# Performance work log

Measured on AMD Instinct MI355X. Metric: run time of the kernel, lower is better.

Reference implementation:

```python
import jax, jax.numpy as jnp
import numpy as np

B, LIN, LOUT = 16, 100, 100
V, D, AD, H, HID = 32000, 512, 64, 8, 2048
RECYCLE, PAD = 1, 0
SCALE = float(np.sqrt(AD))

def _pe(L, dim):
    # positional(pos, i) = pos / 10000 ** ((i//2)/dim); sin on even i, cos on odd i
    pos = jnp.arange(L, dtype=jnp.float32)[:, None]
    i = jnp.arange(dim)
    ang = pos / jnp.power(jnp.float32(10000.0), (i // 2).astype(jnp.float32) / dim)
    return jnp.where(i % 2 == 0, jnp.sin(ang), jnp.cos(ang))  # (L, dim)

def _ln(x, g, b):
    m = x.mean(-1, keepdims=True)
    v = ((x - m) ** 2).mean(-1, keepdims=True)
    return (x - m) / jnp.sqrt(v + 1e-5) * g + b

def _mha(q, k, v, mask, p):
    wq, bq, wk, bk, wv, bv, wo, bo, g, b = p
    m, lq, _ = q.shape
    lk = k.shape[1]
    Q = (q @ wq + bq).reshape(m, lq, H, AD).transpose(0, 2, 1, 3)
    K = (k @ wk + bk).reshape(m, lk, H, AD).transpose(0, 2, 1, 3)
    Vh = (v @ wv + bv).reshape(m, lk, H, AD).transpose(0, 2, 1, 3)
    attn = jnp.einsum('mnld,mnkd->mnlk', Q / SCALE, K)
    attn = jnp.where(mask[:, None, :, :], attn, jnp.float32(-1e9))
    attn = jax.nn.softmax(attn, axis=-1)
    o = jnp.einsum('mnlk,mnkd->mnld', attn, Vh)
    # original uses rearrange 'm n l d -> m l (d n)': d is the OUTER factor
    o = o.transpose(0, 2, 3, 1).reshape(m, lq, AD * H)
    o = o @ wo + bo + q  # dropout is identity in eval
    return _ln(o, g, b)

def _ff(x, w1, b1, w2, b2, g, b):
    return _ln(jax.nn.relu(x @ w1 + b1) @ w2 + b2 + x, g, b)

def _forward(floats, inputs, outputs):
    (sw, fcb,
     ewq, ebq, ewk, ebk, ewv, ebv, ewo, ebo, eg1, eb1, ef1w, ef1b, ef2w, ef2b, eg2, eb2,
     dwq, dbq, dwk, dbk, dwv, dbv, dwo, dbo, dg1, db1, df1w, df1b, df2w, df2b, dg2, db2) = floats
    enc_p = (ewq, ebq, ewk, ebk, ewv, ebv, ewo, ebo, eg1, eb1)
    dec_p = (dwq, dbq, dwk, dbk, dwv, dbv, dwo, dbo, dg1, db1)
    in_mask = (inputs != PAD)[:, None, :]                    # (B,1,LIN) -> bcast (B,1,1,LIN)
    tril = jnp.tril(jnp.ones((LOUT, LOUT), dtype=bool))
    out_mask = (outputs != PAD)[:, None, :] & tril[None]     # (B,LOUT,LOUT)
    enc = sw[inputs] + _pe(LIN, D)[None]
    for _ in range(RECYCLE + 1):  # shared weights reused each iteration
        enc = _mha(enc, enc, enc, in_mask, enc_p)
        enc = _ff(enc, ef1w, ef1b, ef2w, ef2b, eg2, eb2)
    dec = sw[outputs] + _pe(LOUT, D)[None]
    for _ in range(RECYCLE + 1):  # same MHA module for self- and cross-attention
        dec = _mha(dec, dec, dec, out_mask, dec_p)
        dec = _mha(dec, enc, enc, in_mask, dec_p)
        dec = _ff(dec, df1w, df1b, df2w, df2b, dg2, db2)
    dec = dec * jnp.float32(D ** -0.5)
    logits = dec @ sw.T + fcb  # fc.weight tied to share_weight
    return jax.nn.softmax(logits, axis=-1)

def setup_inputs():
    key = jax.random.key(0)
    ks = iter(jax.random.split(key, 64))
    rn = lambda shape: jax.random.normal(next(ks), shape, dtype=jnp.float32) * 0.02
    z = lambda shape: jnp.zeros(shape, jnp.float32)
    o = lambda shape: jnp.ones(shape, jnp.float32)
    d = {'inputs': jax.random.randint(next(ks), (B, LIN), 0, V),
         'outputs': jax.random.randint(next(ks), (B, LOUT), 0, V),
         'share_weight': rn((V, D)), 'fc_b': z((V,))}
    for p in ('enc', 'dec'):
        d[f'{p}_wq'] = rn((D, H * AD)); d[f'{p}_bq'] = z((H * AD,))
        d[f'{p}_wk'] = rn((D, H * AD)); d[f'{p}_bk'] = z((H * AD,))
        d[f'{p}_wv'] = rn((D, H * AD)); d[f'{p}_bv'] = z((H * AD,))
        d[f'{p}_wo'] = rn((H * AD, D)); d[f'{p}_bo'] = z((D,))
        d[f'{p}_g1'] = o((D,)); d[f'{p}_b1'] = z((D,))
        d[f'{p}_f1w'] = rn((D, HID)); d[f'{p}_f1b'] = z((HID,))
        d[f'{p}_f2w'] = rn((HID, D)); d[f'{p}_f2b'] = z((D,))
        d[f'{p}_g2'] = o((D,)); d[f'{p}_b2'] = z((D,))
    return d

def reference(inputs, outputs, share_weight, fc_b, enc_wq, enc_bq, enc_wk, enc_bk, enc_wv, enc_bv, enc_wo, enc_bo, enc_g1, enc_b1, enc_f1w, enc_f1b, enc_f2w, enc_f2b, enc_g2, enc_b2, dec_wq, dec_bq, dec_wk, dec_bk, dec_wv, dec_bv, dec_wo, dec_bo, dec_g1, dec_b1, dec_f1w, dec_f1b, dec_f2w, dec_f2b, dec_g2, dec_b2):
    floats = (share_weight, fc_b, enc_wq, enc_bq, enc_wk, enc_bk, enc_wv, enc_bv, enc_wo, enc_bo, enc_g1, enc_b1, enc_f1w, enc_f1b, enc_f2w, enc_f2b, enc_g2, enc_b2, dec_wq, dec_bq, dec_wk, dec_bk, dec_wv, dec_bv, dec_wo, dec_bo, dec_g1, dec_b1, dec_f1w, dec_f1b, dec_f2w, dec_f2b, dec_g2, dec_b2)
    return _forward(floats, inputs, outputs)
```

## Files before the change

kernel.cpp:

```cpp
#include <hip/hip_runtime.h>

#define TQ     1600
#define MP     1664
#define DM     512
#define NHD    8
#define HD     64
#define VOCAB  32000
#define HID    2048
#define LSEQ   100
#define NSTRIPE 500
#define SCALEV 0.044194173824159216f

typedef unsigned short u16;
typedef unsigned int u32;
typedef __attribute__((ext_vector_type(8))) short bf16x8;
typedef __attribute__((ext_vector_type(4))) float f32x4;

__device__ __forceinline__ u16 f2b(float x) {
  union { float f; unsigned u; } c; c.f = x;
  unsigned r = (c.u + 0x7FFFu + ((c.u >> 16) & 1u)) >> 16;
  return (u16)r;
}
__device__ __forceinline__ float b2f(u16 b) {
  union { unsigned u; float f; } c; c.u = ((unsigned)b) << 16; return c.f;
}
__device__ __forceinline__ unsigned pk2(float lo, float hi) {
  return (unsigned)f2b(lo) | ((unsigned)f2b(hi) << 16);
}
__device__ __forceinline__ float wredsum(float v) {
#pragma unroll
  for (int o = 32; o > 0; o >>= 1) v += __shfl_xor(v, o, 64);
  return v;
}

struct PrepArgs {
  const float* wsrc[12];
  u16* wdst[12];
  int K[12], N[12], toff[12];
  int ntile;
  const float* bsrc[6];
  float* qbE; float* qbD;
};

__global__ __launch_bounds__(256) void prep_kernel(PrepArgs a) {
  __shared__ float t[64][65];
  int bid = blockIdx.x, tid = threadIdx.x;
  if (bid < a.ntile) {
    int wi = 0;
#pragma unroll
    for (int i = 1; i < 12; ++i) if (bid >= a.toff[i]) wi = i;
    int tile = bid - a.toff[wi];
    int K = a.K[wi], N = a.N[wi];
    int ktiles = K >> 6;
    int k0 = (tile % ktiles) << 6, n0 = (tile / ktiles) << 6;
    const float* src = a.wsrc[wi];
    u16* dst = a.wdst[wi];
    int r = tid >> 4, c = (tid & 15) * 4;
#pragma unroll
    for (int i = 0; i < 4; ++i) {
      float4 v = *(const float4*)(src + (size_t)(k0 + r + i * 16) * N + n0 + c);
      t[r + i * 16][c + 0] = v.x; t[r + i * 16][c + 1] = v.y;
      t[r + i * 16][c + 2] = v.z; t[r + i * 16][c + 3] = v.w;
    }
    __syncthreads();
#pragma unroll
    for (int i = 0; i < 4; ++i) {
      int n = r + i * 16;
      ushort4 o;
      o.x = f2b(t[c + 0][n]); o.y = f2b(t[c + 1][n]);
      o.z = f2b(t[c + 2][n]); o.w = f2b(t[c + 3][n]);
      *(ushort4*)(dst + (size_t)(n0 + n) * K + k0 + c) = o;
    }
  } else {
    int j = (bid - a.ntile) * 256 + tid;
    if (j < 3072) {
      int which = j >> 9, o = j & 511;
      float v = a.bsrc[which][o];
      if (which < 3) a.qbE[which * 512 + o] = v;
      else           a.qbD[(which - 3) * 512 + o] = v;
    }
  }
}

__global__ __launch_bounds__(256) void embed_kernel(const int* __restrict__ tokA,
                                                    const int* __restrict__ tokB,
                                                    const float* __restrict__ sw,
                                                    u16* __restrict__ bufA,
                                                    u16* __restrict__ bufB) {
  const int half = MP * DM / 256;
  int bid = blockIdx.x;
  const int* tok = (bid < half) ? tokA : tokB;
  u16* out = (bid < half) ? bufA : bufB;
  int idx = (bid < half ? bid : bid - half) * 256 + threadIdx.x;
  int row = idx >> 9, d = idx & 511;
  float v = 0.f;
  if (row < TQ) {
    int l = row % LSEQ;
    int t = tok[row];
    float freq = expf(-(float)(d >> 1) * (9.210340371976184f / 512.0f));
    float ang = (float)l * freq;
    float pe = (d & 1) ? cosf(ang) : sinf(ang);
    v = sw[(size_t)t * DM + d] + pe;
  }
  out[idx] = f2b(v);
}

template<bool RELU, bool RES>
__global__ __launch_bounds__(256) void bgemm_kernel(
    const u16* __restrict__ A, const u16* __restrict__ BT,
    const float* __restrict__ bias, const u16* __restrict__ res,
    u16* __restrict__ C, int K, int ldc)
{
  __shared__ u16 As[64 * 64];
  __shared__ u16 Bs[64 * 64];
  const int tid = threadIdx.x;
  const int m0 = blockIdx.y << 6, n0 = blockIdx.x << 6;
  const int w = tid >> 6, lane = tid & 63;
  const int c = lane & 15, q = lane >> 4;
  const int srow = tid >> 2, sc = tid & 3;
  const int xr = (srow & 7) << 4;
  const u16* ag = A + (size_t)(m0 + srow) * K + sc * 16;
  const u16* bg = BT + (size_t)(n0 + srow) * K + sc * 16;
  const int arow = w * 16 + c;
  const int axr = (arow & 7) << 4;
  f32x4 acc[4];
#pragma unroll
  for (int t = 0; t < 4; ++t) acc[t] = (f32x4){0.f, 0.f, 0.f, 0.f};

  for (int k0 = 0; k0 < K; k0 += 64) {
    __syncthreads();
    uint4 a0 = *(const uint4*)(ag + k0);
    uint4 a1 = *(const uint4*)(ag + k0 + 8);
    uint4 b0 = *(const uint4*)(bg + k0);
    uint4 b1 = *(const uint4*)(bg + k0 + 8);
    *(uint4*)((char*)As + srow * 128 + ((sc * 32) ^ xr)) = a0;
    *(uint4*)((char*)As + srow * 128 + ((sc * 32 + 16) ^ xr)) = a1;
    *(uint4*)((char*)Bs + srow * 128 + ((sc * 32) ^ xr)) = b0;
    *(uint4*)((char*)Bs + srow * 128 + ((sc * 32 + 16) ^ xr)) = b1;
    __syncthreads();
#pragma unroll
    for (int ks = 0; ks < 2; ++ks) {
      bf16x8 af = *(bf16x8*)((char*)As + arow * 128 + ((ks * 64 + q * 16) ^ axr));
#pragma unroll
      for (int t = 0; t < 4; ++t) {
        int brow = t * 16 + c;
        bf16x8 bf = *(bf16x8*)((char*)Bs + brow * 128 + ((ks * 64 + q * 16) ^ ((brow & 7) << 4)));
        acc[t] = __builtin_amdgcn_mfma_f32_16x16x32_bf16(af, bf, acc[t], 0, 0, 0);
      }
    }
  }
  const int r0 = q * 4;
#pragma unroll
  for (int t = 0; t < 4; ++t) {
    int col = n0 + t * 16 + c;
    float bsv = bias[col];
#pragma unroll
    for (int r = 0; r < 4; ++r) {
      int row = m0 + w * 16 + r0 + r;
      float v = acc[t][r] + bsv;
      if (RES) v += b2f(res[(size_t)row * ldc + col]);
      if (RELU) v = fmaxf(v, 0.f);
      C[(size_t)row * ldc + col] = f2b(v);
    }
  }
}

__global__ __launch_bounds__(256) void ln_kernel(u16* __restrict__ X,
                                                 const float* __restrict__ g,
                                                 const float* __restrict__ b) {
  int row = blockIdx.x * 4 + (threadIdx.x >> 6);
  int lane = threadIdx.x & 63;
  u16* p = X + (size_t)row * DM + lane * 8;
  uint4 u = *(uint4*)p;
  unsigned uu[4] = {u.x, u.y, u.z, u.w};
  float x[8];
#pragma unroll
  for (int e = 0; e < 4; ++e) {
    x[e * 2]     = b2f((u16)(uu[e] & 0xffff));
    x[e * 2 + 1] = b2f((u16)(uu[e] >> 16));
  }
  float s = 0.f;
#pragma unroll
  for (int j = 0; j < 8; ++j) s += x[j];
  s = wredsum(s);
  float mean = s * (1.0f / 512.0f);
  float d2 = 0.f;
#pragma unroll
  for (int j = 0; j < 8; ++j) { float d = x[j] - mean; d2 += d * d; }
  d2 = wredsum(d2);
  float r = rsqrtf(d2 * (1.0f / 512.0f) + 1e-5f);
  const float* gg = g + lane * 8;
  const float* bb = b + lane * 8;
  float y[8];
#pragma unroll
  for (int j = 0; j < 8; ++j) y[j] = (x[j] - mean) * r * gg[j] + bb[j];
  uint4 o;
  o.x = pk2(y[0], y[1]); o.y = pk2(y[2], y[3]);
  o.z = pk2(y[4], y[5]); o.w = pk2(y[6], y[7]);
  *(uint4*)p = o;
}

__global__ __launch_bounds__(256) void attn_kernel(
    const u16* __restrict__ QKV, const int* __restrict__ tok,
    u16* __restrict__ O, int causal)
{
  __shared__ u16 Qs[112 * 64];
  __shared__ u16 Ks[112 * 64];
  __shared__ u16 Vt[64 * 128];
  __shared__ u16 Ps[112 * 128];
  __shared__ int tokv[112];
  int b = blockIdx.x >> 3, h = blockIdx.x & 7;
  int tid = threadIdx.x;

  for (int i = tid; i < 4096; i += 256) ((u32*)Vt)[i] = 0;
  for (int i = tid; i < 7168; i += 256) ((u32*)Ps)[i] = 0;
  if (tid < 112) tokv[tid] = (tid < 100) ? (tok[b * LSEQ + tid] != 0) : 0;
  __syncthreads();

  const size_t rowbase = (size_t)(b * LSEQ) * 1536 + h * 64;
  for (int i = tid; i < 896; i += 256) {
    int r = i >> 3, c8 = i & 7;
    size_t g = rowbase + (size_t)r * 1536 + c8 * 8;
    uint4 q4 = *(const uint4*)(QKV + g);
    uint4 k4 = *(const uint4*)(QKV + g + 512);
    int off = (c8 * 16) ^ ((r & 7) << 4);
    *(uint4*)((char*)Qs + r * 128 + off) = q4;
    *(uint4*)((char*)Ks + r * 128 + off) = k4;
    if (r < LSEQ) {
      union { uint4 u; u16 s[8]; } cv;
      cv.u = *(const uint4*)(QKV + g + 1024);
#pragma unroll
      for (int j = 0; j < 8; ++j) {
        int d = c8 * 8 + j;
        *(u16*)((char*)Vt + d * 256 + ((2 * r) ^ ((d & 7) << 4))) = cv.s[j];
      }
    }
  }
  __syncthreads();

  const int lane = tid & 63, w = tid >> 6;
  const int c = lane & 15, q = lane >> 4;

#pragma unroll
  for (int half = 0; half < 2; ++half) {
    int mt = w + half * 4;
    if (mt > 6) continue;
    f32x4 s[7];
#pragma unroll
    for (int nt = 0; nt < 7; ++nt) s[nt] = (f32x4){0.f, 0.f, 0.f, 0.f};
    int arow = mt * 16 + c;
    int axr = (arow & 7) << 4;
    bf16x8 a0 = *(bf16x8*)((char*)Qs + arow * 128 + ((q * 16) ^ axr));
    bf16x8 a1 = *(bf16x8*)((char*)Qs + arow * 128 + ((64 + q * 16) ^ axr));
#pragma unroll
    for (int nt = 0; nt < 7; ++nt) {
      int brow = nt * 16 + c;
      int bxr = (brow & 7) << 4;
      bf16x8 b0 = *(bf16x8*)((char*)Ks + brow * 128 + ((q * 16) ^ bxr));
      bf16x8 b1 = *(bf16x8*)((char*)Ks + brow * 128 + ((64 + q * 16) ^ bxr));
      s[nt] = __builtin_amdgcn_mfma_f32_16x16x32_bf16(a0, b0, s[nt], 0, 0, 0);
      s[nt] = __builtin_amdgcn_mfma_f32_16x16x32_bf16(a1, b1, s[nt], 0, 0, 0);
    }
#pragma unroll
    for (int r = 0; r < 4; ++r) {
      int mrow = mt * 16 + q * 4 + r;
      float sv[7];
      float mx = -3.0e38f;
#pragma unroll
      for (int nt = 0; nt < 7; ++nt) {
        int kcol = nt * 16 + c;
        float x = s[nt][r];
        bool real = kcol < LSEQ;
        bool ok = real && tokv[kcol] && (!causal || kcol <= mrow);
        x = ok ? x * 0.125f : (real ? -1e9f : -3.0e38f);
        sv[nt] = x;
        mx = fmaxf(mx, x);
      }
#pragma unroll
      for (int o = 1; o < 16; o <<= 1) mx = fmaxf(mx, __shfl_xor(mx, o, 64));
      float sum = 0.f;
#pragma unroll
      for (int nt = 0; nt < 7; ++nt) { sv[nt] = __expf(sv[nt] - mx); sum += sv[nt]; }
#pragma unroll
      for (int o = 1; o < 16; o <<= 1) sum += __shfl_xor(sum, o, 64);
      float inv = 1.0f / sum;
      int pxr = (mrow & 7) << 4;
#pragma unroll
      for (int nt = 0; nt < 7; ++nt) {
        int kcol = nt * 16 + c;
        *(u16*)((char*)Ps + mrow * 256 + ((2 * kcol) ^ pxr)) = f2b(sv[nt] * inv);
      }
    }
    asm volatile("s_waitcnt lgkmcnt(0)" ::: "memory");
    __builtin_amdgcn_sched_barrier(0);
    int prow = mt * 16 + c;
    int pxr2 = (prow & 7) << 4;
    bf16x8 pa[4];
#pragma unroll
    for (int ks = 0; ks < 4; ++ks)
      pa[ks] = *(bf16x8*)((char*)Ps + prow * 256 + ((ks * 64 + q * 16) ^ pxr2));
#pragma unroll
    for (int dt = 0; dt < 4; ++dt) {
      f32x4 o = (f32x4){0.f, 0.f, 0.f, 0.f};
      int vrow = dt * 16 + c;
      int vxr = (vrow & 7) << 4;
#pragma unroll
      for (int ks = 0; ks < 4; ++ks) {
        bf16x8 vb = *(bf16x8*)((char*)Vt + vrow * 256 + ((ks * 64 + q * 16) ^ vxr));
        o = __builtin_amdgcn_mfma_f32_16x16x32_bf16(pa[ks], vb, o, 0, 0, 0);
      }
#pragma unroll
      for (int r = 0; r < 4; ++r) {
        int mrow = mt * 16 + q * 4 + r;
        if (mrow < LSEQ) {
          int d = dt * 16 + c;
          O[(size_t)(b * LSEQ + mrow) * DM + d * 8 + h] = f2b(o[r]);
        }
      }
    }
  }
}

template<bool PART>
__global__ __launch_bounds__(256) void vgemm_kernel(
    const u16* __restrict__ A, const float* __restrict__ sw,
    const float* __restrict__ fcb, float* __restrict__ out,
    float2* __restrict__ pbuf)
{
  __shared__ u16 Bs[64 * 512];
  const int tid = threadIdx.x;
  const int n0 = blockIdx.x << 6;
  for (int i = tid; i < 4096; i += 256) {
    int row = i >> 6, c8 = i & 63;
    const float* s = sw + (size_t)(n0 + row) * DM + c8 * 8;
    float4 f0 = *(const float4*)s;
    float4 f1 = *(const float4*)(s + 4);
    uint4 o;
    o.x = pk2(f0.x, f0.y); o.y = pk2(f0.z, f0.w);
    o.z = pk2(f1.x, f1.y); o.w = pk2(f1.z, f1.w);
    *(uint4*)((char*)Bs + row * 1024 + ((c8 * 16) ^ ((row & 7) << 4))) = o;
  }
  __syncthreads();
  const int w = tid >> 6, lane = tid & 63;
  const int c = lane & 15, q = lane >> 4;
  const u16* pA = A + (size_t)(w * 16 + c) * DM + q * 8;
  float fb[4];
#pragma unroll
  for (int t = 0; t < 4; ++t) fb[t] = fcb[n0 + t * 16 + c];
  for (int mt = 0; mt < 25; ++mt) {
    f32x4 acc[4];
#pragma unroll
    for (int t = 0; t < 4; ++t) acc[t] = (f32x4){0.f, 0.f, 0.f, 0.f};
    size_t moff = (size_t)mt * 64 * DM;
#pragma unroll 4
    for (int ks = 0; ks < 16; ++ks) {
      union { uint4 u; bf16x8 b; } ca;
      ca.u = *(const uint4*)(pA + moff + ks * 32);
#pragma unroll
      for (int t = 0; t < 4; ++t) {
        int brow = t * 16 + c;
        bf16x8 bf = *(bf16x8*)((char*)Bs + brow * 1024 + ((ks * 64 + q * 16) ^ ((brow & 7) << 4)));
        acc[t] = __builtin_amdgcn_mfma_f32_16x16x32_bf16(ca.b, bf, acc[t], 0, 0, 0);
      }
    }
    float lv[4][4];
#pragma unroll
    for (int t = 0; t < 4; ++t)
#pragma unroll
      for (int r = 0; r < 4; ++r) lv[t][r] = acc[t][r] * SCALEV + fb[t];
#pragma unroll
    for (int t = 0; t < 4; ++t) {
      int col = n0 + t * 16 + c;
#pragma unroll
      for (int r = 0; r < 4; ++r) {
        int row = mt * 64 + w * 16 + q * 4 + r;
        out[(size_t)row * VOCAB + col] = lv[t][r];
      }
    }
    if (PART) {
      float pm[4], ps[4];
#pragma unroll
      for (int r = 0; r < 4; ++r) {
        float mx = fmaxf(fmaxf(lv[0][r], lv[1][r]), fmaxf(lv[2][r], lv[3][r]));
#pragma unroll
        for (int o = 1; o < 16; o <<= 1) mx = fmaxf(mx, __shfl_xor(mx, o, 64));
        float ss = 0.f;
#pragma unroll
        for (int t = 0; t < 4; ++t) ss += __expf(lv[t][r] - mx);
#pragma unroll
        for (int o = 1; o < 16; o <<= 1) ss += __shfl_xor(ss, o, 64);
        pm[r] = mx; ps[r] = ss;
      }
      if (c < 4) {
        int row = mt * 64 + w * 16 + q * 4 + c;
        pbuf[(size_t)row * NSTRIPE + blockIdx.x] = make_float2(pm[c], ps[c]);
      }
    }
  }
}

__global__ __launch_bounds__(256) void reduce_partials(const float2* __restrict__ pbuf,
                                                       float2* __restrict__ MS) {
  int row = blockIdx.x * 4 + (threadIdx.x >> 6);
  int lane = threadIdx.x & 63;
  float m = -3.0e38f, s = 0.f;
  for (int i = lane; i < NSTRIPE; i += 64) {
    float2 p = pbuf[(size_t)row * NSTRIPE + i];
    float mn = fmaxf(m, p.x);
    s = s * __expf(m - mn) + p.y * __expf(p.x - mn);
    m = mn;
  }
#pragma unroll
  for (int o = 1; o < 64; o <<= 1) {
    float m2 = __shfl_xor(m, o, 64);
    float s2 = __shfl_xor(s, o, 64);
    float mn = fmaxf(m, m2);
    s = s * __expf(m - mn) + s2 * __expf(m2 - mn);
    m = mn;
  }
  if (lane == 0) MS[row] = make_float2(m, 1.0f / s);
}

__global__ __launch_bounds__(256) void rowstat_kernel(const float* __restrict__ L,
                                                      float2* __restrict__ MS) {
  __shared__ float am[4], as_[4];
  int row = blockIdx.x, tid = threadIdx.x;
  const float* p = L + (size_t)row * VOCAB;
  float m = -3.0e38f, s = 0.f;
  for (int i = tid; i < VOCAB; i += 256) {
    float x = p[i];
    if (x > m) { s *= __expf(m - x); m = x; }
    s += __expf(x - m);
  }
#pragma unroll
  for (int o = 1; o < 64; o <<= 1) {
    float m2 = __shfl_xor(m, o, 64);
    float s2 = __shfl_xor(s, o, 64);
    float mn = fmaxf(m, m2);
    s = s * __expf(m - mn) + s2 * __expf(m2 - mn);
    m = mn;
  }
  if ((tid & 63) == 0) { am[tid >> 6] = m; as_[tid >> 6] = s; }
  __syncthreads();
  if (tid == 0) {
    float M = am[0], S = as_[0];
#pragma unroll
    for (int k = 1; k < 4; ++k) {
      float mn = fmaxf(M, am[k]);
      S = S * __expf(M - mn) + as_[k] * __expf(am[k] - mn);
      M = mn;
    }
    MS[row] = make_float2(M, 1.0f / S);
  }
}

__global__ __launch_bounds__(256) void vfinal_kernel(float* __restrict__ P,
                                                     const float2* __restrict__ MS) {
  int row = blockIdx.y;
  int col = blockIdx.x * 1024 + threadIdx.x * 4;
  if (col >= VOCAB) return;
  float2 ms = MS[row];
  float* p = P + (size_t)row * VOCAB + col;
  float4 x = *(float4*)p;
  x.x = __expf(x.x - ms.x) * ms.y;
  x.y = __expf(x.y - ms.x) * ms.y;
  x.z = __expf(x.z - ms.x) * ms.y;
  x.w = __expf(x.w - ms.x) * ms.y;
  *(float4*)p = x;
}

extern "C" void kernel_launch(void* const* d_in, const int* in_sizes, int n_in,
                              void* d_out, int out_size, void* d_ws, size_t ws_size,
                              hipStream_t stream) {
  (void)in_sizes; (void)n_in; (void)out_size;
  const int* inputs  = (const int*)d_in[0];
  const int* outputs = (const int*)d_in[1];
  const float* sw  = (const float*)d_in[2];
  const float* fcb = (const float*)d_in[3];
  const float* E[16];
  const float* Dd[16];
  for (int i = 0; i < 16; ++i) E[i]  = (const float*)d_in[4 + i];
  for (int i = 0; i < 16; ++i) Dd[i] = (const float*)d_in[20 + i];

  u16* bufE = (u16*)d_ws;
  u16* bufD = bufE + (size_t)MP * DM;
  size_t offMS = (size_t)2 * MP * DM * 2;
  size_t offPB = offMS + (size_t)TQ * 8;
  size_t need  = offPB + (size_t)TQ * NSTRIPE * 8;
  float2* MS   = (float2*)((char*)d_ws + offMS);
  float2* pbuf = (float2*)((char*)d_ws + offPB);
  bool part = ws_size >= need;

  char* base = (char*)d_out;
  size_t off = 0;
  auto carve = [&](size_t bytes) { void* p = base + off; off += (bytes + 255) & ~(size_t)255; return p; };
  u16* bqkvE = (u16*)carve((size_t)MP * 1536 * 2);
  u16* bqkvD = (u16*)carve((size_t)MP * 1536 * 2);
  u16* ba    = (u16*)carve((size_t)MP * DM * 2);
  u16* bh    = (u16*)carve((size_t)MP * HID * 2);
  u16* wqkvE = (u16*)carve((size_t)1536 * 512 * 2);
  u16* woE   = (u16*)carve((size_t)512 * 512 * 2);
  u16* f1E   = (u16*)carve((size_t)2048 * 512 * 2);
  u16* f2E   = (u16*)carve((size_t)512 * 2048 * 2);
  u16* wqkvD = (u16*)carve((size_t)1536 * 512 * 2);
  u16* woD   = (u16*)carve((size_t)512 * 512 * 2);
  u16* f1D   = (u16*)carve((size_t)2048 * 512 * 2);
  u16* f2D   = (u16*)carve((size_t)512 * 2048 * 2);
  float* qbE = (float*)carve(1536 * 4);
  float* qbD = (float*)carve(1536 * 4);
  float* out = (float*)d_out;

  PrepArgs pa;
  const float* ws_[12] = {E[0], E[2], E[4], E[6], E[10], E[12],
                          Dd[0], Dd[2], Dd[4], Dd[6], Dd[10], Dd[12]};
  u16* wd_[12] = {wqkvE, wqkvE + 512 * 512, wqkvE + 1024 * 512, woE, f1E, f2E,
                  wqkvD, wqkvD + 512 * 512, wqkvD + 1024 * 512, woD, f1D, f2D};
  int K_[12] = {512, 512, 512, 512, 512, 2048, 512, 512, 512, 512, 512, 2048};
  int N_[12] = {512, 512, 512, 512, 2048, 512, 512, 512, 512, 512, 2048, 512};
  int tiles = 0;
  for (int i = 0; i < 12; ++i) {
    pa.wsrc[i] = ws_[i]; pa.wdst[i] = wd_[i]; pa.K[i] = K_[i]; pa.N[i] = N_[i];
    pa.toff[i] = tiles;
    tiles += (K_[i] >> 6) * (N_[i] >> 6);
  }
  pa.ntile = tiles;
  const float* bs_[6] = {E[1], E[3], E[5], Dd[1], Dd[3], Dd[5]};
  for (int i = 0; i < 6; ++i) pa.bsrc[i] = bs_[i];
  pa.qbE = qbE; pa.qbD = qbD;
  prep_kernel<<<tiles + 12, 256, 0, stream>>>(pa);

  embed_kernel<<<2 * MP * DM / 256, 256, 0, stream>>>(inputs, outputs, sw, bufE, bufD);

  const dim3 Gqkv(24, 26), G512(8, 26), Gkv(16, 26), Ghid(32, 26);

  for (int it = 0; it < 2; ++it) {
    bgemm_kernel<false,false><<<Gqkv,256,0,stream>>>(bufE, wqkvE, qbE, nullptr, bqkvE, 512, 1536);
    attn_kernel<<<128,256,0,stream>>>(bqkvE, inputs, ba, 0);
    bgemm_kernel<false,true><<<G512,256,0,stream>>>(ba, woE, E[7], bufE, bufE, 512, 512);
    ln_kernel<<<TQ/4,256,0,stream>>>(bufE, E[8], E[9]);
    bgemm_kernel<true,false><<<Ghid,256,0,stream>>>(bufE, f1E, E[11], nullptr, bh, 512, 2048);
    bgemm_kernel<false,true><<<G512,256,0,stream>>>(bh, f2E, E[13], bufE, bufE, 2048, 512);
    ln_kernel<<<TQ/4,256,0,stream>>>(bufE, E[14], E[15]);
  }
  for (int it = 0; it < 2; ++it) {
    bgemm_kernel<false,false><<<Gqkv,256,0,stream>>>(bufD, wqkvD, qbD, nullptr, bqkvD, 512, 1536);
    attn_kernel<<<128,256,0,stream>>>(bqkvD, outputs, ba, 1);
    bgemm_kernel<false,true><<<G512,256,0,stream>>>(ba, woD, Dd[7], bufD, bufD, 512, 512);
    ln_kernel<<<TQ/4,256,0,stream>>>(bufD, Dd[8], Dd[9]);
    bgemm_kernel<false,false><<<G512,256,0,stream>>>(bufD, wqkvD, qbD, nullptr, bqkvD, 512, 1536);
    bgemm_kernel<false,false><<<Gkv,256,0,stream>>>(bufE, wqkvD + 512 * 512, qbD + 512, nullptr, bqkvD + 512, 512, 1536);
    attn_kernel<<<128,256,0,stream>>>(bqkvD, inputs, ba, 0);
    bgemm_kernel<false,true><<<G512,256,0,stream>>>(ba, woD, Dd[7], bufD, bufD, 512, 512);
    ln_kernel<<<TQ/4,256,0,stream>>>(bufD, Dd[8], Dd[9]);
    bgemm_kernel<true,false><<<Ghid,256,0,stream>>>(bufD, f1D, Dd[11], nullptr, bh, 512, 2048);
    bgemm_kernel<false,true><<<G512,256,0,stream>>>(bh, f2D, Dd[13], bufD, bufD, 2048, 512);
    ln_kernel<<<TQ/4,256,0,stream>>>(bufD, Dd[14], Dd[15]);
  }

  if (part) {
    vgemm_kernel<true><<<NSTRIPE, 256, 0, stream>>>(bufD, sw, fcb, out, pbuf);
    reduce_partials<<<TQ / 4, 256, 0, stream>>>(pbuf, MS);
  } else {
    vgemm_kernel<false><<<NSTRIPE, 256, 0, stream>>>(bufD, sw, fcb, out, nullptr);
    rowstat_kernel<<<TQ, 256, 0, stream>>>(out, MS);
  }
  vfinal_kernel<<<dim3(32, TQ), 256, 0, stream>>>(out, MS);
}
```

Baseline: 587.8 us.

## Retile GEMMs, split attention by query half, and recompute vocab logits for softmax

Several changes at once. Large GEMMs get a 128-row tile template. Attention launches twice as many blocks, each handling half the queries. The decoder cross-attention K/V projection of the encoder output is hoisted out of the decoder loop, and the positional table is precomputed in the prep kernel. The vocab projection now processes five row tiles per pass, and in partial mode it recomputes the logits in a second pass that writes the softmax directly, replacing the fp32 logits write plus the separate normalize kernel. The recompute doubles the vocab GEMM's arithmetic in exchange for dropping a full read-modify-write of the large output.

```diff
diff --git a/kernel.cpp b/kernel.cpp
--- a/kernel.cpp
+++ b/kernel.cpp
@@ -39,7 +39,7 @@
   int K[12], N[12], toff[12];
   int ntile;
   const float* bsrc[6];
-  float* qbE; float* qbD;
+  float* qbE; float* qbD; float* peT;
 };
 
 __global__ __launch_bounds__(256) void prep_kernel(PrepArgs a) {
@@ -71,7 +71,7 @@
       o.z = f2b(t[c + 2][n]); o.w = f2b(t[c + 3][n]);
       *(ushort4*)(dst + (size_t)(n0 + n) * K + k0 + c) = o;
     }
-  } else {
+  } else if (bid < a.ntile + 12) {
     int j = (bid - a.ntile) * 256 + tid;
     if (j < 3072) {
       int which = j >> 9, o = j & 511;
@@ -79,12 +79,21 @@
       if (which < 3) a.qbE[which * 512 + o] = v;
       else           a.qbD[(which - 3) * 512 + o] = v;
     }
+  } else {
+    int idx = (bid - a.ntile - 12) * 256 + tid;
+    if (idx < LSEQ * 512) {
+      int l = idx >> 9, d = idx & 511;
+      float freq = expf(-(float)(d >> 1) * (9.210340371976184f / 512.0f));
+      float ang = (float)l * freq;
+      a.peT[idx] = (d & 1) ? cosf(ang) : sinf(ang);
+    }
   }
 }
 
 __global__ __launch_bounds__(256) void embed_kernel(const int* __restrict__ tokA,
                                                     const int* __restrict__ tokB,
                                                     const float* __restrict__ sw,
+                                                    const float* __restrict__ peT,
                                                     u16* __restrict__ bufA,
                                                     u16* __restrict__ bufB) {
   const int half = MP * DM / 256;
@@ -97,67 +106,74 @@
   if (row < TQ) {
     int l = row % LSEQ;
     int t = tok[row];
-    float freq = expf(-(float)(d >> 1) * (9.210340371976184f / 512.0f));
-    float ang = (float)l * freq;
-    float pe = (d & 1) ? cosf(ang) : sinf(ang);
-    v = sw[(size_t)t * DM + d] + pe;
+    v = sw[(size_t)t * DM + d] + peT[l * 512 + d];
   }
   out[idx] = f2b(v);
 }
 
-template<bool RELU, bool RES>
+template<int MT, bool RELU, bool RES>
 __global__ __launch_bounds__(256) void bgemm_kernel(
     const u16* __restrict__ A, const u16* __restrict__ BT,
     const float* __restrict__ bias, const u16* __restrict__ res,
     u16* __restrict__ C, int K, int ldc)
 {
-  __shared__ u16 As[64 * 64];
+  __shared__ u16 As[64 * MT * 64];
   __shared__ u16 Bs[64 * 64];
   const int tid = threadIdx.x;
-  const int m0 = blockIdx.y << 6, n0 = blockIdx.x << 6;
+  const int m0 = blockIdx.y * (64 * MT), n0 = blockIdx.x << 6;
   const int w = tid >> 6, lane = tid & 63;
   const int c = lane & 15, q = lane >> 4;
-  const int srow = tid >> 2, sc = tid & 3;
-  const int xr = (srow & 7) << 4;
-  const u16* ag = A + (size_t)(m0 + srow) * K + sc * 16;
-  const u16* bg = BT + (size_t)(n0 + srow) * K + sc * 16;
-  const int arow = w * 16 + c;
-  const int axr = (arow & 7) << 4;
-  f32x4 acc[4];
-#pragma unroll
-  for (int t = 0; t < 4; ++t) acc[t] = (f32x4){0.f, 0.f, 0.f, 0.f};
+  const int tr = tid >> 3, tc = tid & 7;
+  const int sbase = tr * 128 + ((tc * 16) ^ ((tr & 7) << 4));
+  const u16* agp = A + (size_t)(m0 + tr) * K + tc * 8;
+  const u16* bgp = BT + (size_t)(n0 + tr) * K + tc * 8;
+  f32x4 acc[MT][4];
+#pragma unroll
+  for (int i = 0; i < MT; ++i)
+#pragma unroll
+    for (int t = 0; t < 4; ++t) acc[i][t] = (f32x4){0.f, 0.f, 0.f, 0.f};
 
   for (int k0 = 0; k0 < K; k0 += 64) {
     __syncthreads();
-    uint4 a0 = *(const uint4*)(ag + k0);
-    uint4 a1 = *(const uint4*)(ag + k0 + 8);
-    uint4 b0 = *(const uint4*)(bg + k0);
-    uint4 b1 = *(const uint4*)(bg + k0 + 8);
-    *(uint4*)((char*)As + srow * 128 + ((sc * 32) ^ xr)) = a0;
-    *(uint4*)((char*)As + srow * 128 + ((sc * 32 + 16) ^ xr)) = a1;
-    *(uint4*)((char*)Bs + srow * 128 + ((sc * 32) ^ xr)) = b0;
-    *(uint4*)((char*)Bs + srow * 128 + ((sc * 32 + 16) ^ xr)) = b1;
+#pragma unroll
+    for (int rep = 0; rep < 2 * MT; ++rep) {
+      uint4 v = *(const uint4*)(agp + k0 + (size_t)rep * 32 * K);
+      *(uint4*)((char*)As + sbase + rep * 4096) = v;
+    }
+#pragma unroll
+    for (int rep = 0; rep < 2; ++rep) {
+      uint4 v = *(const uint4*)(bgp + k0 + (size_t)rep * 32 * K);
+      *(uint4*)((char*)Bs + sbase + rep * 4096) = v;
+    }
     __syncthreads();
 #pragma unroll
     for (int ks = 0; ks < 2; ++ks) {
-      bf16x8 af = *(bf16x8*)((char*)As + arow * 128 + ((ks * 64 + q * 16) ^ axr));
+      bf16x8 af[MT];
+#pragma unroll
+      for (int i = 0; i < MT; ++i) {
+        int arow = w * 16 * MT + i * 16 + c;
+        af[i] = *(bf16x8*)((char*)As + arow * 128 + ((ks * 64 + q * 16) ^ ((arow & 7) << 4)));
+      }
 #pragma unroll
       for (int t = 0; t < 4; ++t) {
         int brow = t * 16 + c;
         bf16x8 bf = *(bf16x8*)((char*)Bs + brow * 128 + ((ks * 64 + q * 16) ^ ((brow & 7) << 4)));
-        acc[t] = __builtin_amdgcn_mfma_f32_16x16x32_bf16(af, bf, acc[t], 0, 0, 0);
-      }
-    }
-  }
-  const int r0 = q * 4;
+#pragma unroll
+        for (int i = 0; i < MT; ++i)
+          acc[i][t] = __builtin_amdgcn_mfma_f32_16x16x32_bf16(af[i], bf, acc[i][t], 0, 0, 0);
+      }
+    }
+  }
+#pragma unroll
+  for (int i = 0; i < MT; ++i)
 #pragma unroll
   for (int t = 0; t < 4; ++t) {
     int col = n0 + t * 16 + c;
     float bsv = bias[col];
 #pragma unroll
     for (int r = 0; r < 4; ++r) {
-      int row = m0 + w * 16 + r0 + r;
-      float v = acc[t][r] + bsv;
+      int row = m0 + w * 16 * MT + i * 16 + q * 4 + r;
+      float v = acc[i][t][r] + bsv;
       if (RES) v += b2f(res[(size_t)row * ldc + col]);
       if (RELU) v = fmaxf(v, 0.f);
       C[(size_t)row * ldc + col] = f2b(v);
@@ -204,16 +220,17 @@
     const u16* __restrict__ QKV, const int* __restrict__ tok,
     u16* __restrict__ O, int causal)
 {
-  __shared__ u16 Qs[112 * 64];
+  __shared__ u16 Qs[64 * 64];
   __shared__ u16 Ks[112 * 64];
   __shared__ u16 Vt[64 * 128];
-  __shared__ u16 Ps[112 * 128];
+  __shared__ u16 Ps[64 * 128];
   __shared__ int tokv[112];
-  int b = blockIdx.x >> 3, h = blockIdx.x & 7;
+  int bid = blockIdx.x;
+  int b = bid >> 4, h = (bid >> 1) & 7, half = bid & 1;
   int tid = threadIdx.x;
 
   for (int i = tid; i < 4096; i += 256) ((u32*)Vt)[i] = 0;
-  for (int i = tid; i < 7168; i += 256) ((u32*)Ps)[i] = 0;
+  for (int i = tid; i < 4096; i += 256) ((u32*)Ps)[i] = 0;
   if (tid < 112) tokv[tid] = (tid < 100) ? (tok[b * LSEQ + tid] != 0) : 0;
   __syncthreads();
 
@@ -221,11 +238,13 @@
   for (int i = tid; i < 896; i += 256) {
     int r = i >> 3, c8 = i & 7;
     size_t g = rowbase + (size_t)r * 1536 + c8 * 8;
-    uint4 q4 = *(const uint4*)(QKV + g);
+    int off = (c8 * 16) ^ ((r & 7) << 4);
     uint4 k4 = *(const uint4*)(QKV + g + 512);
-    int off = (c8 * 16) ^ ((r & 7) << 4);
-    *(uint4*)((char*)Qs + r * 128 + off) = q4;
     *(uint4*)((char*)Ks + r * 128 + off) = k4;
+    if (r < 64) {
+      uint4 q4 = *(const uint4*)(QKV + g + (size_t)(half * 64) * 1536);
+      *(uint4*)((char*)Qs + r * 128 + off) = q4;
+    }
     if (r < LSEQ) {
       union { uint4 u; u16 s[8]; } cv;
       cv.u = *(const uint4*)(QKV + g + 1024);
@@ -240,11 +259,9 @@
 
   const int lane = tid & 63, w = tid >> 6;
   const int c = lane & 15, q = lane >> 4;
-
-#pragma unroll
-  for (int half = 0; half < 2; ++half) {
-    int mt = w + half * 4;
-    if (mt > 6) continue;
+  const int mt = w;
+  const int mbase = half * 64 + mt * 16;
+  if (mbase < 112) {
     f32x4 s[7];
 #pragma unroll
     for (int nt = 0; nt < 7; ++nt) s[nt] = (f32x4){0.f, 0.f, 0.f, 0.f};
@@ -263,7 +280,8 @@
     }
 #pragma unroll
     for (int r = 0; r < 4; ++r) {
-      int mrow = mt * 16 + q * 4 + r;
+      int mrow = mbase + q * 4 + r;
+      int ml = mt * 16 + q * 4 + r;
       float sv[7];
       float mx = -3.0e38f;
 #pragma unroll
@@ -284,11 +302,11 @@
 #pragma unroll
       for (int o = 1; o < 16; o <<= 1) sum += __shfl_xor(sum, o, 64);
       float inv = 1.0f / sum;
-      int pxr = (mrow & 7) << 4;
+      int pxr = (ml & 7) << 4;
 #pragma unroll
       for (int nt = 0; nt < 7; ++nt) {
         int kcol = nt * 16 + c;
-        *(u16*)((char*)Ps + mrow * 256 + ((2 * kcol) ^ pxr)) = f2b(sv[nt] * inv);
+        *(u16*)((char*)Ps + ml * 256 + ((2 * kcol) ^ pxr)) = f2b(sv[nt] * inv);
       }
     }
     asm volatile("s_waitcnt lgkmcnt(0)" ::: "memory");
@@ -311,7 +329,7 @@
       }
 #pragma unroll
       for (int r = 0; r < 4; ++r) {
-        int mrow = mt * 16 + q * 4 + r;
+        int mrow = mbase + q * 4 + r;
         if (mrow < LSEQ) {
           int d = dt * 16 + c;
           O[(size_t)(b * LSEQ + mrow) * DM + d * 8 + h] = f2b(o[r]);
@@ -321,11 +339,11 @@
   }
 }
 
-template<bool PART>
+template<int MODE>
 __global__ __launch_bounds__(256) void vgemm_kernel(
     const u16* __restrict__ A, const float* __restrict__ sw,
     const float* __restrict__ fcb, float* __restrict__ out,
-    float2* __restrict__ pbuf)
+    float2* __restrict__ pbuf, const float2* __restrict__ MS)
 {
   __shared__ u16 Bs[64 * 512];
   const int tid = threadIdx.x;
@@ -343,57 +361,75 @@
   __syncthreads();
   const int w = tid >> 6, lane = tid & 63;
   const int c = lane & 15, q = lane >> 4;
-  const u16* pA = A + (size_t)(w * 16 + c) * DM + q * 8;
   float fb[4];
 #pragma unroll
   for (int t = 0; t < 4; ++t) fb[t] = fcb[n0 + t * 16 + c];
-  for (int mt = 0; mt < 25; ++mt) {
-    f32x4 acc[4];
-#pragma unroll
-    for (int t = 0; t < 4; ++t) acc[t] = (f32x4){0.f, 0.f, 0.f, 0.f};
-    size_t moff = (size_t)mt * 64 * DM;
+
+  for (int g = 0; g < 5; ++g) {
+    f32x4 acc[5][4];
+#pragma unroll
+    for (int j = 0; j < 5; ++j)
+#pragma unroll
+      for (int t = 0; t < 4; ++t) acc[j][t] = (f32x4){0.f, 0.f, 0.f, 0.f};
+    const u16* pA = A + (size_t)(g * 320 + w * 16 + c) * DM + q * 8;
 #pragma unroll 4
     for (int ks = 0; ks < 16; ++ks) {
-      union { uint4 u; bf16x8 b; } ca;
-      ca.u = *(const uint4*)(pA + moff + ks * 32);
+      union { uint4 u; bf16x8 b; } ca[5];
+#pragma unroll
+      for (int j = 0; j < 5; ++j)
+        ca[j].u = *(const uint4*)(pA + (size_t)j * 64 * DM + ks * 32);
 #pragma unroll
       for (int t = 0; t < 4; ++t) {
         int brow = t * 16 + c;
         bf16x8 bf = *(bf16x8*)((char*)Bs + brow * 1024 + ((ks * 64 + q * 16) ^ ((brow & 7) << 4)));
-        acc[t] = __builtin_amdgcn_mfma_f32_16x16x32_bf16(ca.b, bf, acc[t], 0, 0, 0);
-      }
-    }
-    float lv[4][4];
-#pragma unroll
-    for (int t = 0; t < 4; ++t)
-#pragma unroll
-      for (int r = 0; r < 4; ++r) lv[t][r] = acc[t][r] * SCALEV + fb[t];
-#pragma unroll
-    for (int t = 0; t < 4; ++t) {
-      int col = n0 + t * 16 + c;
-#pragma unroll
-      for (int r = 0; r < 4; ++r) {
-        int row = mt * 64 + w * 16 + q * 4 + r;
-        out[(size_t)row * VOCAB + col] = lv[t][r];
-      }
-    }
-    if (PART) {
-      float pm[4], ps[4];
-#pragma unroll
-      for (int r = 0; r < 4; ++r) {
-        float mx = fmaxf(fmaxf(lv[0][r], lv[1][r]), fmaxf(lv[2][r], lv[3][r]));
-#pragma unroll
-        for (int o = 1; o < 16; o <<= 1) mx = fmaxf(mx, __shfl_xor(mx, o, 64));
-        float ss = 0.f;
-#pragma unroll
-        for (int t = 0; t < 4; ++t) ss += __expf(lv[t][r] - mx);
-#pragma unroll
-        for (int o = 1; o < 16; o <<= 1) ss += __shfl_xor(ss, o, 64);
-        pm[r] = mx; ps[r] = ss;
-      }
-      if (c < 4) {
-        int row = mt * 64 + w * 16 + q * 4 + c;
-        pbuf[(size_t)row * NSTRIPE + blockIdx.x] = make_float2(pm[c], ps[c]);
+#pragma unroll
+        for (int j = 0; j < 5; ++j)
+          acc[j][t] = __builtin_amdgcn_mfma_f32_16x16x32_bf16(ca[j].b, bf, acc[j][t], 0, 0, 0);
+      }
+    }
+#pragma unroll
+    for (int j = 0; j < 5; ++j) {
+      int row0 = g * 320 + j * 64 + w * 16 + q * 4;
+      float lv[4][4];
+#pragma unroll
+      for (int t = 0; t < 4; ++t)
+#pragma unroll
+        for (int r = 0; r < 4; ++r) lv[t][r] = acc[j][t][r] * SCALEV + fb[t];
+      if (MODE == 0) {
+        float pm[4], ps[4];
+#pragma unroll
+        for (int r = 0; r < 4; ++r) {
+          float mx = fmaxf(fmaxf(lv[0][r], lv[1][r]), fmaxf(lv[2][r], lv[3][r]));
+#pragma unroll
+          for (int o = 1; o < 16; o <<= 1) mx = fmaxf(mx, __shfl_xor(mx, o, 64));
+          float ss = 0.f;
+#pragma unroll
+          for (int t = 0; t < 4; ++t) ss += __expf(lv[t][r] - mx);
+#pragma unroll
+          for (int o = 1; o < 16; o <<= 1) ss += __shfl_xor(ss, o, 64);
+          pm[r] = mx; ps[r] = ss;
+        }
+        if (c < 4)
+          pbuf[(size_t)(row0 + c) * NSTRIPE + blockIdx.x] = make_float2(pm[c], ps[c]);
+      } else if (MODE == 1) {
+        float2 msv[4];
+#pragma unroll
+        for (int r = 0; r < 4; ++r) msv[r] = MS[row0 + r];
+#pragma unroll
+        for (int t = 0; t < 4; ++t) {
+          int col = n0 + t * 16 + c;
+#pragma unroll
+          for (int r = 0; r < 4; ++r)
+            out[(size_t)(row0 + r) * VOCAB + col] = __expf(lv[t][r] - msv[r].x) * msv[r].y;
+        }
+      } else {
+#pragma unroll
+        for (int t = 0; t < 4; ++t) {
+          int col = n0 + t * 16 + c;
+#pragma unroll
+          for (int r = 0; r < 4; ++r)
+            out[(size_t)(row0 + r) * VOCAB + col] = lv[t][r];
+        }
       }
     }
   }
@@ -508,6 +544,7 @@
   u16* f2D   = (u16*)carve((size_t)512 * 2048 * 2);
   float* qbE = (float*)carve(1536 * 4);
   float* qbD = (float*)carve(1536 * 4);
+  float* peT = (float*)carve((size_t)LSEQ * 512 * 4);
   float* out = (float*)d_out;
 
   PrepArgs pa;
@@ -526,43 +563,44 @@
   pa.ntile = tiles;
   const float* bs_[6] = {E[1], E[3], E[5], Dd[1], Dd[3], Dd[5]};
   for (int i = 0; i < 6; ++i) pa.bsrc[i] = bs_[i];
-  pa.qbE = qbE; pa.qbD = qbD;
-  prep_kernel<<<tiles + 12, 256, 0, stream>>>(pa);
-
-  embed_kernel<<<2 * MP * DM / 256, 256, 0, stream>>>(inputs, outputs, sw, bufE, bufD);
-
-  const dim3 Gqkv(24, 26), G512(8, 26), Gkv(16, 26), Ghid(32, 26);
+  pa.qbE = qbE; pa.qbD = qbD; pa.peT = peT;
+  prep_kernel<<<tiles + 12 + 200, 256, 0, stream>>>(pa);
+
+  embed_kernel<<<2 * MP * DM / 256, 256, 0, stream>>>(inputs, outputs, sw, peT, bufE, bufD);
+
+  const dim3 GqkvM2(24, 13), G512(8, 26), Gkv(16, 26), GhidM2(32, 13);
 
   for (int it = 0; it < 2; ++it) {
-    bgemm_kernel<false,false><<<Gqkv,256,0,stream>>>(bufE, wqkvE, qbE, nullptr, bqkvE, 512, 1536);
-    attn_kernel<<<128,256,0,stream>>>(bqkvE, inputs, ba, 0);
-    bgemm_kernel<false,true><<<G512,256,0,stream>>>(ba, woE, E[7], bufE, bufE, 512, 512);
+    bgemm_kernel<2,false,false><<<GqkvM2,256,0,stream>>>(bufE, wqkvE, qbE, nullptr, bqkvE, 512, 1536);
+    attn_kernel<<<256,256,0,stream>>>(bqkvE, inputs, ba, 0);
+    bgemm_kernel<1,false,true><<<G512,256,0,stream>>>(ba, woE, E[7], bufE, bufE, 512, 512);
     ln_kernel<<<TQ/4,256,0,stream>>>(bufE, E[8], E[9]);
-    bgemm_kernel<true,false><<<Ghid,256,0,stream>>>(bufE, f1E, E[11], nullptr, bh, 512, 2048);
-    bgemm_kernel<false,true><<<G512,256,0,stream>>>(bh, f2E, E[13], bufE, bufE, 2048, 512);
+    bgemm_kernel<2,true,false><<<GhidM2,256,0,stream>>>(bufE, f1E, E[11], nullptr, bh, 512, 2048);
+    bgemm_kernel<1,false,true><<<G512,256,0,stream>>>(bh, f2E, E[13], bufE, bufE, 2048, 512);
     ln_kernel<<<TQ/4,256,0,stream>>>(bufE, E[14], E[15]);
   }
+  bgemm_kernel<1,false,false><<<Gkv,256,0,stream>>>(bufE, wqkvD + 512 * 512, qbD + 512, nullptr, bqkvD + 512, 512, 1536);
   for (int it = 0; it < 2; ++it) {
-    bgemm_kernel<false,false><<<Gqkv,256,0,stream>>>(bufD, wqkvD, qbD, nullptr, bqkvD, 512, 1536);
-    attn_kernel<<<128,256,0,stream>>>(bqkvD, outputs, ba, 1);
-    bgemm_kernel<false,true><<<G512,256,0,stream>>>(ba, woD, Dd[7], bufD, bufD, 512, 512);
+    bgemm_kernel<2,false,false><<<GqkvM2,256,0,stream>>>(bufD, wqkvD, qbD, nullptr, bqkvE, 512, 1536);
+    attn_kernel<<<256,256,0,stream>>>(bqkvE, outputs, ba, 1);
+    bgemm_kernel<1,false,true><<<G512,256,0,stream>>>(ba, woD, Dd[7], bufD, bufD, 512, 512);
     ln_kernel<<<TQ/4,256,0,stream>>>(bufD, Dd[8], Dd[9]);
-    bgemm_kernel<false,false><<<G512,256,0,stream>>>(bufD, wqkvD, qbD, nullptr, bqkvD, 512, 1536);
-    bgemm_kernel<false,false><<<Gkv,256,0,stream>>>(bufE, wqkvD + 512 * 512, qbD + 512, nullptr, bqkvD + 512, 512, 1536);
-    attn_kernel<<<128,256,0,stream>>>(bqkvD, inputs, ba, 0);
-    bgemm_kernel<false,true><<<G512,256,0,stream>>>(ba, woD, Dd[7], bufD, bufD, 512, 512);
+    bgemm_kernel<1,false,false><<<G512,256,0,stream>>>(bufD, wqkvD, qbD, nullptr, bqkvD, 512, 1536);
+    attn_kernel<<<256,256,0,stream>>>(bqkvD, inputs, ba, 0);
+    bgemm_kernel<1,false,true><<<G512,256,0,stream>>>(ba, woD, Dd[7], bufD, bufD, 512, 512);
     ln_kernel<<<TQ/4,256,0,stream>>>(bufD, Dd[8], Dd[9]);
-    bgemm_kernel<true,false><<<Ghid,256,0,stream>>>(bufD, f1D, Dd[11], nullptr, bh, 512, 2048);
-    bgemm_kernel<false,true><<<G512,256,0,stream>>>(bh, f2D, Dd[13], bufD, bufD, 2048, 512);
+    bgemm_kernel<2,true,false><<<GhidM2,256,0,stream>>>(bufD, f1D, Dd[11], nullptr, bh, 512, 2048);
+    bgemm_kernel<1,false,true><<<G512,256,0,stream>>>(bh, f2D, Dd[13], bufD, bufD, 2048, 512);
     ln_kernel<<<TQ/4,256,0,stream>>>(bufD, Dd[14], Dd[15]);
   }
 
   if (part) {
-    vgemm_kernel<true><<<NSTRIPE, 256, 0, stream>>>(bufD, sw, fcb, out, pbuf);
+    vgemm_kernel<0><<<NSTRIPE, 256, 0, stream>>>(bufD, sw, fcb, nullptr, pbuf, nullptr);
     reduce_partials<<<TQ / 4, 256, 0, stream>>>(pbuf, MS);
+    vgemm_kernel<1><<<NSTRIPE, 256, 0, stream>>>(bufD, sw, fcb, out, nullptr, MS);
   } else {
-    vgemm_kernel<false><<<NSTRIPE, 256, 0, stream>>>(bufD, sw, fcb, out, nullptr);
+    vgemm_kernel<2><<<NSTRIPE, 256, 0, stream>>>(bufD, sw, fcb, out, nullptr, nullptr);
     rowstat_kernel<<<TQ, 256, 0, stream>>>(out, MS);
-  }
-  vfinal_kernel<<<dim3(32, TQ), 256, 0, stream>>>(out, MS);
-}
+    vfinal_kernel<<<dim3(32, TQ), 256, 0, stream>>>(out, MS);
+  }
+}
```

After: 770.0 us. 31.0% more time.
